# Performance work log

Measured on AMD Instinct MI355X. Metric: run time of the kernel, lower is better.

The kernel has to match this reference:

```python
import jax, jax.numpy as jnp
import numpy as np
from jax import lax

EPS = 1e-5  # BatchNorm / LayerNorm eps
B, DIM, H, W = 32, 256, 64, 64
S = 64            # state_dim
D_INNER = 256     # ssd_expand * dim
HIDDEN = 1024     # mlp_ratio * dim


def _bn(x, g, b, m, v):
    # BatchNorm2d, inference mode with given running stats. x: (B,C,H,W)
    inv = lax.rsqrt(v + EPS)
    return (x - m[None, :, None, None]) * (g * inv)[None, :, None, None] + b[None, :, None, None]


def _dwconv3x3(x, w):
    # depthwise 3x3 conv, stride 1, SAME padding. w: (C,1,3,3)
    return lax.conv_general_dilated(
        x, w, window_strides=(1, 1), padding='SAME',
        feature_group_count=x.shape[1],
        dimension_numbers=('NCHW', 'OIHW', 'NCHW'))


def setup_inputs() -> dict:
    key = jax.random.key(0)
    ks = jax.random.split(key, 32)
    n = lambda i, shp, s=0.02: jax.random.normal(ks[i], shp, jnp.float32) * s
    u = lambda i, shp: jax.random.uniform(ks[i], shp, jnp.float32)
    return {
        'x': jax.random.normal(ks[0], (B, DIM, H, W), jnp.float32),
        # dwconv1 (Conv2dNorm depthwise)
        'dw1_w': n(1, (DIM, 1, 3, 3)), 'dw1_g': 1.0 + n(2, (DIM,)), 'dw1_b': n(3, (DIM,)),
        'dw1_m': n(4, (DIM,)), 'dw1_v': u(5, (DIM,)) + 0.5,
        # LayerNorm1d
        'ln_w': 1.0 + n(6, (DIM,)), 'ln_b': n(7, (DIM,)),
        # mixer (HSMSSD)
        'bcdt_w': n(8, (3 * S, DIM)),
        'dwm_w': n(9, (3 * S, 1, 3, 3)),
        'A_param': 1.0 + 15.0 * u(10, (S,)),
        'hz_w': n(11, (2 * D_INNER, DIM)),
        'out_w': n(12, (DIM, D_INNER)),
        'D_param': jnp.ones((1,), jnp.float32),
        # dwconv2
        'dw2_w': n(13, (DIM, 1, 3, 3)), 'dw2_g': 1.0 + n(14, (DIM,)), 'dw2_b': n(15, (DIM,)),
        'dw2_m': n(16, (DIM,)), 'dw2_v': u(17, (DIM,)) + 0.5,
        # FFN
        'fc1_w': n(18, (HIDDEN, DIM)), 'fc1_g': 1.0 + n(19, (HIDDEN,)), 'fc1_b': n(20, (HIDDEN,)),
        'fc1_m': n(21, (HIDDEN,)), 'fc1_v': u(22, (HIDDEN,)) + 0.5,
        'fc2_w': n(23, (DIM, HIDDEN)), 'fc2_g': 1.0 + n(24, (DIM,)), 'fc2_b': n(25, (DIM,)),
        'fc2_m': n(26, (DIM,)), 'fc2_v': u(27, (DIM,)) + 0.5,
        # alpha-gated residual blends
        'alpha': 1e-4 * jnp.ones((4, DIM), jnp.float32) + n(28, (4, DIM), 0.01),
    }


def reference(x, dw1_w, dw1_g, dw1_b, dw1_m, dw1_v, ln_w, ln_b,
              bcdt_w, dwm_w, A_param, hz_w, out_w, D_param,
              dw2_w, dw2_g, dw2_b, dw2_m, dw2_v,
              fc1_w, fc1_g, fc1_b, fc1_m, fc1_v,
              fc2_w, fc2_g, fc2_b, fc2_m, fc2_v, alpha):
    b, dim, h_, w_ = x.shape
    L = h_ * w_
    a = jax.nn.sigmoid(alpha)[:, :, None, None]  # (4, dim, 1, 1)

    # alpha-blended depthwise conv 1
    x = (1.0 - a[0]) * x + a[0] * _bn(_dwconv3x3(x, dw1_w), dw1_g, dw1_b, dw1_m, dw1_v)
    x_prev = x

    # LayerNorm1d over channel dim on (B, C, L)
    xf = x.reshape(b, dim, L)
    mean = xf.mean(axis=1, keepdims=True)
    var = ((xf - mean) ** 2).mean(axis=1, keepdims=True)
    xn = (xf - mean) * lax.rsqrt(var + EPS) * ln_w[None, :, None] + ln_b[None, :, None]

    # HSMSSD mixer
    bc_dt = jnp.einsum('bcl,oc->bol', xn, bcdt_w).reshape(b, 3 * S, h_, w_)
    bc_dt = _dwconv3x3(bc_dt, dwm_w).reshape(b, 3 * S, L)
    Bm, Cm, dt = jnp.split(bc_dt, 3, axis=1)          # each (B, S, L)
    Am = jax.nn.softmax(dt + A_param[None, :, None], axis=-1)
    AB = Am * Bm                                      # (B, S, L)
    h = jnp.einsum('bcl,bsl->bcs', xn, AB)            # (B, dim, S)
    hz = jnp.einsum('bcs,oc->bos', h, hz_w)           # (B, 2*d_inner, S)
    hh, z = jnp.split(hz, 2, axis=1)
    hg = hh * jax.nn.silu(z) + hh * D_param[0]
    hout = jnp.einsum('bcs,oc->bos', hg, out_w)       # (B, dim, S)
    y = jnp.einsum('bcs,bsl->bcl', hout, Cm).reshape(b, dim, h_, w_)

    x = (1.0 - a[1]) * x_prev + a[1] * y
    x = (1.0 - a[2]) * x + a[2] * _bn(_dwconv3x3(x, dw2_w), dw2_g, dw2_b, dw2_m, dw2_v)

    # FFN: 1x1 conv + BN + ReLU + 1x1 conv + BN
    t = _bn(jnp.einsum('bchw,oc->bohw', x, fc1_w), fc1_g, fc1_b, fc1_m, fc1_v)
    t = jax.nn.relu(t)
    t = _bn(jnp.einsum('bchw,oc->bohw', t, fc2_w), fc2_g, fc2_b, fc2_m, fc2_v)
    x = (1.0 - a[3]) * x + a[3] * t
    return (x, hout)
```

## Files before the change

### kernel.cpp

```cpp
#include <hip/hip_runtime.h>
#include <hip/hip_bf16.h>

typedef __hip_bfloat16 bf16;
typedef __attribute__((ext_vector_type(8))) short bf16x8;
typedef __attribute__((ext_vector_type(4))) float f32x4;

__device__ __forceinline__ float LD(const float* p){ return *p; }
__device__ __forceinline__ float LD(const bf16* p){ return __bfloat162float(*p); }
__device__ __forceinline__ void ST(float* p, float v){ *p = v; }
__device__ __forceinline__ void ST(bf16* p, float v){ *p = __float2bfloat16(v); }
__device__ __forceinline__ float sigm(float v){ return 1.f/(1.f + expf(-v)); }
__device__ __forceinline__ ushort f2b(float f){
    unsigned u = __float_as_uint(f);
    return (ushort)((u + 0x7fffu + ((u>>16)&1u)) >> 16);
}

#define NEPS 1e-5f

__device__ __forceinline__ void stage_tile(const float* __restrict__ xp, float* tile, int tid){
    for (int i = tid; i < 66*66; i += 256) {
        int r = i/66, c = i%66;
        int gr = r-1, gc = c-1;
        float val = 0.f;
        if (gr >= 0 && gr < 64 && gc >= 0 && gc < 64) val = xp[gr*64+gc];
        tile[i] = val;
    }
}
__device__ __forceinline__ void stage_tile(const bf16* __restrict__ xp, float* tile, int tid){
    for (int i = tid; i < 2048; i += 256) {
        int r = i >> 5, c = (i & 31) << 1;
        uint u = *(const uint*)((const ushort*)xp + r*64 + c);
        tile[(r+1)*66 + c+1] = __uint_as_float(u << 16);
        tile[(r+1)*66 + c+2] = __uint_as_float(u & 0xffff0000u);
    }
    for (int i = tid; i < 260; i += 256) {
        int tr, tc;
        if (i < 66)       { tr = 0;      tc = i; }
        else if (i < 132) { tr = 65;     tc = i-66; }
        else if (i < 196) { tr = i-131;  tc = 0; }
        else              { tr = i-195;  tc = 65; }
        tile[tr*66 + tc] = 0.f;
    }
}
__device__ __forceinline__ void st_pair(float* op, int idx, float a, float b){
    op[idx] = a; op[idx+1] = b;
}
__device__ __forceinline__ void st_pair(bf16* op, int idx, float a, float b){
    uint u = (uint)f2b(a) | ((uint)f2b(b)<<16);
    *(uint*)((ushort*)op + idx) = u;
}

template<typename TIN, typename TOUT>
__global__ __launch_bounds__(256) void dwconv_bn_blend(
        const TIN* __restrict__ xin, TOUT* __restrict__ xout,
        const float* __restrict__ w, const float* __restrict__ gg, const float* __restrict__ bb,
        const float* __restrict__ mm, const float* __restrict__ vv,
        const float* __restrict__ alpha, int arow)
{
    __shared__ float tile[66*66];
    int blk = blockIdx.x;
    int ch = blk & 255;
    const TIN* xp = xin + (size_t)blk*4096;
    TOUT* op = xout + (size_t)blk*4096;
    int tid = threadIdx.x;
    stage_tile(xp, tile, tid);
    __syncthreads();
    float wv[9];
    #pragma unroll
    for (int k=0;k<9;k++) wv[k] = w[ch*9+k];
    float sc = gg[ch] * rsqrtf(vv[ch] + NEPS);
    float mv = mm[ch], bv = bb[ch];
    float av = sigm(alpha[arow*256+ch]);
    for (int p2 = tid; p2 < 2048; p2 += 256) {
        int r = p2 >> 5, c = (p2 & 31) << 1;
        float a0 = 0.f, a1 = 0.f;
        #pragma unroll
        for (int dr=0;dr<3;dr++)
            #pragma unroll
            for (int dc=0;dc<3;dc++){
                float wk = wv[dr*3+dc];
                a0 += wk*tile[(r+dr)*66 + c+dc];
                a1 += wk*tile[(r+dr)*66 + c+1+dc];
            }
        float bn0 = (a0 - mv)*sc + bv;
        float bn1 = (a1 - mv)*sc + bv;
        float xv0 = tile[(r+1)*66 + c+1];
        float xv1 = tile[(r+1)*66 + c+2];
        st_pair(op, r*64+c, (1.f-av)*xv0 + av*bn0, (1.f-av)*xv1 + av*bn1);
    }
}

template<typename TX>
__global__ __launch_bounds__(256) void ln_stats(const TX* __restrict__ x1,
        float* __restrict__ meanp, float* __restrict__ invp)
{
    int blk = blockIdx.x;
    int b = blk >> 4;
    int l = ((blk & 15) << 8) + threadIdx.x;
    const TX* xp = x1 + (size_t)b*256*4096 + l;
    float mean = 0.f, m2 = 0.f;
    for (int c=0;c<256;c++){ float v = LD(&xp[(size_t)c*4096]); mean += v; m2 += v*v; }
    mean *= (1.f/256.f); m2 *= (1.f/256.f);
    meanp[b*4096 + l] = mean;
    invp[b*4096 + l] = rsqrtf(m2 - mean*mean + NEPS);
}

__global__ __launch_bounds__(256) void prep_k(
        const float* __restrict__ f1w, const float* __restrict__ f2w,
        const float* __restrict__ bcdtw,
        const float* __restrict__ g1, const float* __restrict__ b1,
        const float* __restrict__ m1, const float* __restrict__ v1,
        const float* __restrict__ g2, const float* __restrict__ b2,
        const float* __restrict__ m2, const float* __restrict__ v2,
        ushort* __restrict__ w1bf, ushort* __restrict__ w2bf,
        ushort* __restrict__ wbc,
        float* __restrict__ sc1, float* __restrict__ sb1,
        float* __restrict__ sc2, float* __restrict__ sb2)
{
    int i = blockIdx.x*256 + threadIdx.x;
    if (i < 262144) {
        w1bf[i] = f2b(f1w[i]);
        w2bf[i] = f2b(f2w[i]);
    }
    if (i < 49152) wbc[i] = f2b(bcdtw[i]);
    if (i < 1024) { float s = g1[i]*rsqrtf(v1[i]+NEPS); sc1[i]=s; sb1[i]=b1[i]-m1[i]*s; }
    if (i < 256)  { float s = g2[i]*rsqrtf(v2[i]+NEPS); sc2[i]=s; sb2[i]=b2[i]-m2[i]*s; }
}

template<typename TX>
__global__ __launch_bounds__(256) void bcdt_mfma(
        const TX* __restrict__ x1,
        const float* __restrict__ meanp, const float* __restrict__ invp,
        const float* __restrict__ lnw, const float* __restrict__ lnb,
        const ushort* __restrict__ wbc,
        bf16* __restrict__ bc, ushort* __restrict__ xn_bf, int b0)
{
    __shared__ __align__(16) ushort Xs[64*256];
    int blk = blockIdx.x;
    int lb = blk >> 6;
    int b  = b0 + lb;
    int l0 = (blk & 63) << 6;
    int tid = threadIdx.x, lane = tid & 63, w = tid >> 6;
    const TX* xp = x1 + (size_t)b*256*4096 + l0;
    float mval = meanp[b*4096 + l0 + lane];
    float ival = invp [b*4096 + l0 + lane];
    ushort* xnp = xn_bf + (size_t)lb*256*4096 + l0;

    for (int cc = w*8; cc < 256; cc += 32) {
        ushort u[8];
        #pragma unroll
        for (int j=0;j<8;j++){
            float v = LD(&xp[(size_t)(cc+j)*4096 + lane]);
            float xn = (v - mval)*ival*lnw[cc+j] + lnb[cc+j];
            u[j] = f2b(xn);
            xnp[(size_t)(cc+j)*4096 + lane] = u[j];
        }
        uint4 pk;
        pk.x = (uint)u[0] | ((uint)u[1]<<16);
        pk.y = (uint)u[2] | ((uint)u[3]<<16);
        pk.z = (uint)u[4] | ((uint)u[5]<<16);
        pk.w = (uint)u[6] | ((uint)u[7]<<16);
        int g = (cc>>3) ^ (lane&7);
        *(uint4*)&Xs[lane*256 + g*8] = pk;
    }
    __syncthreads();

    f32x4 zero4 = {0.f,0.f,0.f,0.f};
    f32x4 acc[3][4];
    #pragma unroll
    for (int m=0;m<3;m++)
        #pragma unroll
        for (int f=0;f<4;f++) acc[m][f] = zero4;

    int hbase = w*48;
    #pragma unroll
    for (int ks=0; ks<8; ks++){
        bf16x8 afr[3];
        #pragma unroll
        for (int m=0;m<3;m++)
            afr[m] = *(const bf16x8*)&wbc[(size_t)(hbase + m*16 + (lane&15))*256
                                          + ks*32 + (lane>>4)*8];
        #pragma unroll
        for (int f=0;f<4;f++){
            int px = f*16 + (lane&15);
            int g = (ks*4 + (lane>>4)) ^ (px&7);
            bf16x8 bfr = *(const bf16x8*)&Xs[px*256 + g*8];
            #pragma unroll
            for (int m=0;m<3;m++)
                acc[m][f] = __builtin_amdgcn_mfma_f32_16x16x32_bf16(afr[m], bfr, acc[m][f], 0,0,0);
        }
    }
    bf16* op = bc + (size_t)lb*192*4096 + l0;
    #pragma unroll
    for (int m=0;m<3;m++)
        #pragma unroll
        for (int r=0;r<4;r++){
            int o = hbase + m*16 + (lane>>4)*4 + r;
            #pragma unroll
            for (int f=0;f<4;f++){
                int px = f*16 + (lane&15);
                op[(size_t)o*4096 + px] = __float2bfloat16(acc[m][f][r]);
            }
        }
}

__global__ __launch_bounds__(256) void dwconv_plain(bf16* __restrict__ data, const float* __restrict__ w)
{
    __shared__ float tile[66*66];
    int blk = blockIdx.x;
    int ch = blk % 192;
    bf16* xp = data + (size_t)blk*4096;
    int tid = threadIdx.x;
    stage_tile(xp, tile, tid);
    __syncthreads();
    float wv[9];
    #pragma unroll
    for (int k=0;k<9;k++) wv[k] = w[ch*9+k];
    for (int p2 = tid; p2 < 2048; p2 += 256) {
        int r = p2 >> 5, c = (p2 & 31) << 1;
        float a0 = 0.f, a1 = 0.f;
        #pragma unroll
        for (int dr=0;dr<3;dr++)
            #pragma unroll
            for (int dc=0;dc<3;dc++){
                float wk = wv[dr*3+dc];
                a0 += wk*tile[(r+dr)*66 + c+dc];
                a1 += wk*tile[(r+dr)*66 + c+1+dc];
            }
        st_pair(xp, r*64+c, a0, a1);
    }
}

__global__ __launch_bounds__(256) void softmax_ab(bf16* __restrict__ bc, const float* __restrict__ A)
{
    __shared__ float red[8];
    int blk = blockIdx.x;
    int lb = blk >> 6;
    int s = blk & 63;
    bf16* dtp = bc + ((size_t)lb*192 + 128 + s)*4096;
    bf16* bmp = bc + ((size_t)lb*192 + s)*4096;
    int tid = threadIdx.x;
    float Av = A[s];
    float vals[16];
    float mx = -1e30f;
    #pragma unroll
    for (int i=0;i<16;i++){ vals[i] = LD(&dtp[i*256+tid]) + Av; mx = fmaxf(mx, vals[i]); }
    #pragma unroll
    for (int o=32;o>0;o>>=1) mx = fmaxf(mx, __shfl_down(mx, o));
    int lane = tid & 63, wid = tid >> 6;
    if (lane == 0) red[wid] = mx;
    __syncthreads();
    if (tid == 0) red[4] = fmaxf(fmaxf(red[0],red[1]), fmaxf(red[2],red[3]));
    __syncthreads();
    mx = red[4];
    float sum = 0.f;
    #pragma unroll
    for (int i=0;i<16;i++){ vals[i] = expf(vals[i]-mx); sum += vals[i]; }
    #pragma unroll
    for (int o=32;o>0;o>>=1) sum += __shfl_down(sum, o);
    if (lane == 0) red[wid] = sum;
    __syncthreads();
    if (tid == 0) red[5] = red[0]+red[1]+red[2]+red[3];
    __syncthreads();
    float inv = 1.f/red[5];
    #pragma unroll
    for (int i=0;i<16;i++){
        float ab = vals[i]*inv*LD(&bmp[i*256+tid]);
        ST(&bmp[i*256+tid], ab);
    }
}

__global__ __launch_bounds__(256) void h_mfma(
        const ushort* __restrict__ xn_bf, const bf16* __restrict__ bc,
        float* __restrict__ h_part)
{
    int blk = blockIdx.x;
    int lb = blk >> 3;
    int kz = blk & 7;
    int kbase = kz*512;
    int tid = threadIdx.x, lane = tid & 63, w = tid >> 6;
    const ushort* ap = xn_bf + (size_t)lb*256*4096;
    const ushort* bp = (const ushort*)bc + (size_t)lb*192*4096;
    f32x4 zero4 = {0.f,0.f,0.f,0.f};
    f32x4 acc[4][4];
    #pragma unroll
    for (int m=0;m<4;m++)
        #pragma unroll
        for (int n=0;n<4;n++) acc[m][n] = zero4;

    for (int ks=0; ks<16; ks++){
        int koff = kbase + ks*32 + (lane>>4)*8;
        bf16x8 afr[4], bfr[4];
        #pragma unroll
        for (int m=0;m<4;m++)
            afr[m] = *(const bf16x8*)&ap[(size_t)(w*64 + m*16 + (lane&15))*4096 + koff];
        #pragma unroll
        for (int n=0;n<4;n++)
            bfr[n] = *(const bf16x8*)&bp[(size_t)(n*16 + (lane&15))*4096 + koff];
        #pragma unroll
        for (int m=0;m<4;m++)
            #pragma unroll
            for (int n=0;n<4;n++)
                acc[m][n] = __builtin_amdgcn_mfma_f32_16x16x32_bf16(afr[m], bfr[n], acc[m][n], 0,0,0);
    }
    float* hp = h_part + ((size_t)lb*8 + kz)*16384;
    #pragma unroll
    for (int m=0;m<4;m++)
        #pragma unroll
        for (int n=0;n<4;n++)
            #pragma unroll
            for (int r=0;r<4;r++){
                int c = w*64 + m*16 + (lane>>4)*4 + r;
                int s = n*16 + (lane&15);
                hp[c*64 + s] = acc[m][n][r];
            }
}

__global__ __launch_bounds__(256) void hz_gate(const float* __restrict__ h_part,
        const float* __restrict__ w, const float* __restrict__ Dp,
        float* __restrict__ hg)
{
    __shared__ float ht[256][64];
    int blk = blockIdx.x; int lb = blk>>2; int o0 = (blk&3)*64;
    int tid = threadIdx.x;
    const float* hp = h_part + (size_t)lb*8*16384;
    for (int i=tid;i<16384;i+=256){
        float s = 0.f;
        #pragma unroll
        for (int k=0;k<8;k++) s += hp[k*16384 + i];
        ht[i>>6][i&63] = s;
    }
    __syncthreads();
    int lane=tid&63, g=tid>>6;
    float Dv = Dp[0];
    for (int i4=0;i4<4;i4++){
        int ol = o0 + g*16 + i4*4;
        const float* r0 = w + (size_t)ol*256;
        const float *r1=r0+256, *r2=r0+512, *r3=r0+768;
        const float* z0 = w + (size_t)(ol+256)*256;
        const float *z1=z0+256, *z2=z0+512, *z3=z0+768;
        float d0=0.f,d1=0.f,d2=0.f,d3=0.f;
        float e0=0.f,e1=0.f,e2=0.f,e3=0.f;
        #pragma unroll 4
        for (int c4=0;c4<64;c4++){
            float x0=ht[c4*4][lane],x1v=ht[c4*4+1][lane],x2v=ht[c4*4+2][lane],x3v=ht[c4*4+3][lane];
            float4 a0=((const float4*)r0)[c4],a1=((const float4*)r1)[c4];
            float4 a2=((const float4*)r2)[c4],a3=((const float4*)r3)[c4];
            d0 += a0.x*x0+a0.y*x1v+a0.z*x2v+a0.w*x3v;
            d1 += a1.x*x0+a1.y*x1v+a1.z*x2v+a1.w*x3v;
            d2 += a2.x*x0+a2.y*x1v+a2.z*x2v+a2.w*x3v;
            d3 += a3.x*x0+a3.y*x1v+a3.z*x2v+a3.w*x3v;
            float4 b0=((const float4*)z0)[c4],b1=((const float4*)z1)[c4];
            float4 b2=((const float4*)z2)[c4],b3=((const float4*)z3)[c4];
            e0 += b0.x*x0+b0.y*x1v+b0.z*x2v+b0.w*x3v;
            e1 += b1.x*x0+b1.y*x1v+b1.z*x2v+b1.w*x3v;
            e2 += b2.x*x0+b2.y*x1v+b2.z*x2v+b2.w*x3v;
            e3 += b3.x*x0+b3.y*x1v+b3.z*x2v+b3.w*x3v;
        }
        float s0 = e0/(1.f+expf(-e0)) + Dv;
        float s1 = e1/(1.f+expf(-e1)) + Dv;
        float s2 = e2/(1.f+expf(-e2)) + Dv;
        float s3 = e3/(1.f+expf(-e3)) + Dv;
        size_t base = ((size_t)lb*256 + ol)*64 + lane;
        hg[base]=d0*s0; hg[base+64]=d1*s1; hg[base+128]=d2*s2; hg[base+192]=d3*s3;
    }
}

__global__ __launch_bounds__(256) void out_gemm(const float* __restrict__ hg, const float* __restrict__ w,
        ushort* __restrict__ hout_bf, float* __restrict__ hout_out, int b0)
{
    __shared__ float ht[256][64];
    int blk = blockIdx.x; int lb = blk>>2; int b = b0 + lb; int o0 = (blk&3)*64;
    int tid = threadIdx.x;
    const float* hp = hg + (size_t)lb*16384;
    for (int i=tid;i<16384;i+=256) ht[i>>6][i&63]=hp[i];
    __syncthreads();
    int lane=tid&63, g=tid>>6;
    for (int i4=0;i4<4;i4++){
        int ol = g*16 + i4*4;
        const float* r0 = w + (size_t)(o0+ol)*256;
        const float *r1=r0+256, *r2=r0+512, *r3=r0+768;
        float d0=0.f,d1=0.f,d2=0.f,d3=0.f;
        #pragma unroll 8
        for (int c4=0;c4<64;c4++){
            float x0=ht[c4*4][lane],x1v=ht[c4*4+1][lane],x2v=ht[c4*4+2][lane],x3v=ht[c4*4+3][lane];
            float4 a0=((const float4*)r0)[c4],a1=((const float4*)r1)[c4];
            float4 a2=((const float4*)r2)[c4],a3=((const float4*)r3)[c4];
            d0 += a0.x*x0+a0.y*x1v+a0.z*x2v+a0.w*x3v;
            d1 += a1.x*x0+a1.y*x1v+a1.z*x2v+a1.w*x3v;
            d2 += a2.x*x0+a2.y*x1v+a2.z*x2v+a2.w*x3v;
            d3 += a3.x*x0+a3.y*x1v+a3.z*x2v+a3.w*x3v;
        }
        size_t lbase = ((size_t)lb*256 + o0 + ol)*64 + lane;
        hout_bf[lbase]=f2b(d0); hout_bf[lbase+64]=f2b(d1);
        hout_bf[lbase+128]=f2b(d2); hout_bf[lbase+192]=f2b(d3);
        size_t gbase = ((size_t)b*256 + o0 + ol)*64 + lane;
        hout_out[gbase]=d0; hout_out[gbase+64]=d1;
        hout_out[gbase+128]=d2; hout_out[gbase+192]=d3;
    }
}

template<typename TX>
__global__ __launch_bounds__(256) void y_mfma(
        const ushort* __restrict__ hout_bf, const bf16* __restrict__ bc,
        TX* __restrict__ x1, const float* __restrict__ alpha, int b0)
{
    __shared__ __align__(16) ushort Cs[64*64];
    int blk = blockIdx.x; int lb = blk>>6; int b = b0 + lb; int l0 = (blk&63)<<6;
    int tid = threadIdx.x, lane = tid&63, w = tid>>6;
    const ushort* cp = (const ushort*)bc + ((size_t)lb*192 + 64)*4096 + l0;
    for (int sc = w*8; sc < 64; sc += 32){
        ushort u[8];
        #pragma unroll
        for (int j=0;j<8;j++) u[j] = cp[(size_t)(sc+j)*4096 + lane];
        uint4 pk;
        pk.x = (uint)u[0] | ((uint)u[1]<<16);
        pk.y = (uint)u[2] | ((uint)u[3]<<16);
        pk.z = (uint)u[4] | ((uint)u[5]<<16);
        pk.w = (uint)u[6] | ((uint)u[7]<<16);
        int g = (sc>>3) ^ (lane&7);
        *(uint4*)&Cs[lane*64 + g*8] = pk;
    }
    __syncthreads();

    f32x4 zero4 = {0.f,0.f,0.f,0.f};
    f32x4 acc[4][4];
    #pragma unroll
    for (int m=0;m<4;m++)
        #pragma unroll
        for (int f=0;f<4;f++) acc[m][f] = zero4;

    const ushort* ap = hout_bf + (size_t)lb*256*64;
    #pragma unroll
    for (int ks=0; ks<2; ks++){
        bf16x8 afr[4];
        #pragma unroll
        for (int m=0;m<4;m++)
            afr[m] = *(const bf16x8*)&ap[(size_t)(w*64 + m*16 + (lane&15))*64
                                          + ks*32 + (lane>>4)*8];
        #pragma unroll
        for (int f=0;f<4;f++){
            int px = f*16 + (lane&15);
            int s8 = ks*32 + (lane>>4)*8;
            int g = (s8>>3) ^ (px&7);
            bf16x8 bfr = *(const bf16x8*)&Cs[px*64 + g*8];
            #pragma unroll
            for (int m=0;m<4;m++)
                acc[m][f] = __builtin_amdgcn_mfma_f32_16x16x32_bf16(afr[m], bfr, acc[m][f], 0,0,0);
        }
    }

    TX* xpo = x1 + (size_t)b*256*4096 + l0;
    #pragma unroll
    for (int m=0;m<4;m++)
        #pragma unroll
        for (int r=0;r<4;r++){
            int c = w*64 + m*16 + (lane>>4)*4 + r;
            float av = sigm(alpha[256+c]);
            #pragma unroll
            for (int f=0;f<4;f++){
                int px = f*16 + (lane&15);
                float xv = LD(&xpo[(size_t)c*4096 + px]);
                ST(&xpo[(size_t)c*4096 + px], (1.f-av)*xv + av*acc[m][f][r]);
            }
        }
}

template<typename TX>
__global__ __launch_bounds__(256) void ffn_mfma(
        const TX* __restrict__ x,
        const ushort* __restrict__ w1bf,
        const ushort* __restrict__ w2bf,
        const float* __restrict__ sc1, const float* __restrict__ sb1,
        const float* __restrict__ sc2, const float* __restrict__ sb2,
        const float* __restrict__ alpha,
        float* __restrict__ out)
{
    __shared__ __align__(16) ushort Xs[64*256];
    __shared__ __align__(16) ushort Ts[64*128];
    int blk = blockIdx.x;
    int b = blk >> 6, l0 = (blk & 63) << 6;
    int tid = threadIdx.x, lane = tid & 63, w = tid >> 6;
    const TX* xp = x + (size_t)b*256*4096 + l0;

    for (int cc = w*8; cc < 256; cc += 32) {
        float v[8];
        #pragma unroll
        for (int j=0;j<8;j++) v[j] = LD(&xp[(size_t)(cc+j)*4096 + lane]);
        uint4 pk;
        pk.x = (uint)f2b(v[0]) | ((uint)f2b(v[1])<<16);
        pk.y = (uint)f2b(v[2]) | ((uint)f2b(v[3])<<16);
        pk.z = (uint)f2b(v[4]) | ((uint)f2b(v[5])<<16);
        pk.w = (uint)f2b(v[6]) | ((uint)f2b(v[7])<<16);
        int g = (cc>>3) ^ (lane&7);
        *(uint4*)&Xs[lane*256 + g*8] = pk;
    }
    __syncthreads();

    f32x4 zero4 = {0.f,0.f,0.f,0.f};
    f32x4 acc2[4][4];
    #pragma unroll
    for (int m=0;m<4;m++)
        #pragma unroll
        for (int f=0;f<4;f++) acc2[m][f] = zero4;

    for (int hc = 0; hc < 1024; hc += 128) {
        int hbase = hc + w*32;
        f32x4 c1[2][4];
        #pragma unroll
        for (int m=0;m<2;m++)
            #pragma unroll
            for (int f=0;f<4;f++) c1[m][f] = zero4;
        for (int ks = 0; ks < 8; ks++) {
            bf16x8 afr[2];
            #pragma unroll
            for (int m=0;m<2;m++)
                afr[m] = *(const bf16x8*)&w1bf[(size_t)(hbase + m*16 + (lane&15))*256
                                               + ks*32 + (lane>>4)*8];
            #pragma unroll
            for (int f=0;f<4;f++){
                int px = f*16 + (lane&15);
                int g = (ks*4 + (lane>>4)) ^ (px&7);
                bf16x8 bfr = *(const bf16x8*)&Xs[px*256 + g*8];
                #pragma unroll
                for (int m=0;m<2;m++)
                    c1[m][f] = __builtin_amdgcn_mfma_f32_16x16x32_bf16(afr[m], bfr, c1[m][f], 0,0,0);
            }
        }
        __syncthreads();
        #pragma unroll
        for (int m=0;m<2;m++){
            #pragma unroll
            for (int r=0;r<4;r++){
                int h = hbase + m*16 + (lane>>4)*4 + r;
                float s1 = sc1[h], bb1 = sb1[h];
                int hl = h - hc;
                #pragma unroll
                for (int f=0;f<4;f++){
                    int px = f*16 + (lane&15);
                    float t = fmaxf(c1[m][f][r]*s1 + bb1, 0.f);
                    int g = (hl>>3) ^ (px&7);
                    Ts[px*128 + g*8 + (hl&7)] = f2b(t);
                }
            }
        }
        __syncthreads();
        int c0 = w*64;
        for (int ks = 0; ks < 4; ks++) {
            bf16x8 afr[4];
            #pragma unroll
            for (int m=0;m<4;m++)
                afr[m] = *(const bf16x8*)&w2bf[(size_t)(c0 + m*16 + (lane&15))*1024
                                               + hc + ks*32 + (lane>>4)*8];
            #pragma unroll
            for (int f=0;f<4;f++){
                int px = f*16 + (lane&15);
                int hl = ks*32 + (lane>>4)*8;
                int g = (hl>>3) ^ (px&7);
                bf16x8 bfr = *(const bf16x8*)&Ts[px*128 + g*8];
                #pragma unroll
                for (int m=0;m<4;m++)
                    acc2[m][f] = __builtin_amdgcn_mfma_f32_16x16x32_bf16(afr[m], bfr, acc2[m][f], 0,0,0);
            }
        }
    }

    float* op = out + (size_t)b*256*4096 + l0;
    int c0 = w*64;
    #pragma unroll
    for (int m=0;m<4;m++){
        #pragma unroll
        for (int r=0;r<4;r++){
            int c = c0 + m*16 + (lane>>4)*4 + r;
            float a = sigm(alpha[768+c]);
            float s2 = sc2[c], bb2 = sb2[c];
            #pragma unroll
            for (int f=0;f<4;f++){
                int px = f*16 + (lane&15);
                float t2 = acc2[m][f][r]*s2 + bb2;
                float xv = LD(&xp[(size_t)c*4096 + px]);
                op[(size_t)c*4096 + px] = (1.f-a)*xv + a*t2;
            }
        }
    }
}

template<typename TX>
static void run_all(const float* x, TX* x1, float* d_out_x, float* hout_out,
                    const float* dw1w, const float* dw1g, const float* dw1b,
                    const float* dw1m, const float* dw1v,
                    const float* lnw, const float* lnb,
                    const ushort* wbc, const float* dwmw, const float* Ap,
                    const float* hzw, const float* outw, const float* Dp,
                    const float* dw2w, const float* dw2g, const float* dw2b,
                    const float* dw2m, const float* dw2v,
                    const ushort* w1bf, const ushort* w2bf,
                    const float* sc1, const float* sb1,
                    const float* sc2, const float* sb2,
                    const float* alpha,
                    float* meanp, float* invp, char* cbase, int NB,
                    hipStream_t stream)
{
    bf16*   bc      = (bf16*)cbase;
    ushort* xn_bf   = (ushort*)(cbase + (size_t)NB*1572864);
    float*  h_part  = (float*)(cbase + (size_t)NB*(1572864 + 2097152));
    float*  hg      = (float*)((char*)h_part + (size_t)NB*524288);
    ushort* hout_bf = (ushort*)((char*)hg + (size_t)NB*65536);

    dwconv_bn_blend<float,TX><<<8192,256,0,stream>>>(x, x1, dw1w,dw1g,dw1b,dw1m,dw1v, alpha, 0);
    ln_stats<TX><<<512,256,0,stream>>>(x1, meanp, invp);

    for (int b0 = 0; b0 < 32; b0 += NB) {
        bcdt_mfma<TX><<<NB*64,256,0,stream>>>(x1, meanp, invp, lnw, lnb, wbc, bc, xn_bf, b0);
        dwconv_plain<<<NB*192,256,0,stream>>>(bc, dwmw);
        softmax_ab<<<NB*64,256,0,stream>>>(bc, Ap);
        h_mfma<<<NB*8,256,0,stream>>>(xn_bf, bc, h_part);
        hz_gate<<<NB*4,256,0,stream>>>(h_part, hzw, Dp, hg);
        out_gemm<<<NB*4,256,0,stream>>>(hg, outw, hout_bf, hout_out, b0);
        y_mfma<TX><<<NB*64,256,0,stream>>>(hout_bf, bc, x1, alpha, b0);
    }

    dwconv_bn_blend<TX,TX><<<8192,256,0,stream>>>(x1, x1, dw2w,dw2g,dw2b,dw2m,dw2v, alpha, 2);
    ffn_mfma<TX><<<2048,256,0,stream>>>(x1, w1bf, w2bf, sc1, sb1, sc2, sb2, alpha, d_out_x);
}

extern "C" void kernel_launch(void* const* d_in, const int* in_sizes, int n_in,
                              void* d_out, int out_size, void* d_ws, size_t ws_size,
                              hipStream_t stream)
{
    (void)in_sizes; (void)n_in; (void)out_size;
    const float* x     = (const float*)d_in[0];
    const float* dw1w  = (const float*)d_in[1];
    const float* dw1g  = (const float*)d_in[2];
    const float* dw1b  = (const float*)d_in[3];
    const float* dw1m  = (const float*)d_in[4];
    const float* dw1v  = (const float*)d_in[5];
    const float* lnw   = (const float*)d_in[6];
    const float* lnb   = (const float*)d_in[7];
    const float* bcdtw = (const float*)d_in[8];
    const float* dwmw  = (const float*)d_in[9];
    const float* Ap    = (const float*)d_in[10];
    const float* hzw   = (const float*)d_in[11];
    const float* outw  = (const float*)d_in[12];
    const float* Dp    = (const float*)d_in[13];
    const float* dw2w  = (const float*)d_in[14];
    const float* dw2g  = (const float*)d_in[15];
    const float* dw2b  = (const float*)d_in[16];
    const float* dw2m  = (const float*)d_in[17];
    const float* dw2v  = (const float*)d_in[18];
    const float* f1w   = (const float*)d_in[19];
    const float* f1g   = (const float*)d_in[20];
    const float* f1b   = (const float*)d_in[21];
    const float* f1m   = (const float*)d_in[22];
    const float* f1v   = (const float*)d_in[23];
    const float* f2w   = (const float*)d_in[24];
    const float* f2g   = (const float*)d_in[25];
    const float* f2b_  = (const float*)d_in[26];
    const float* f2m   = (const float*)d_in[27];
    const float* f2v   = (const float*)d_in[28];
    const float* alpha = (const float*)d_in[29];

    const size_t nx = (size_t)32*256*4096;
    float* d_out_x  = (float*)d_out;
    float* hout_out = d_out_x + nx;

    char* ws = (char*)d_ws;
    float* meanp = (float*)ws;
    float* invp  = meanp + 131072;
    size_t off = 1048576;
    ushort* w1bf = (ushort*)(ws + off); off += 524288;
    ushort* w2bf = (ushort*)(ws + off); off += 524288;
    ushort* wbc  = (ushort*)(ws + off); off += 98304;
    float* sc1 = (float*)(ws + off); off += 4096;
    float* sb1 = (float*)(ws + off); off += 4096;
    float* sc2 = (float*)(ws + off); off += 1024;
    float* sb2 = (float*)(ws + off); off += 1024;
    off = (off + 255) & ~(size_t)255;

    const size_t perb = 1572864 + 2097152 + 524288 + 65536 + 32768;
    size_t avail = ws_size > off ? ws_size - off : 0;

    prep_k<<<1024,256,0,stream>>>(f1w, f2w, bcdtw, f1g,f1b,f1m,f1v, f2g,f2b_,f2m,f2v,
                                  w1bf, w2bf, wbc, sc1, sb1, sc2, sb2);

    if (avail >= nx*2 + 8*perb) {
        bf16* x1b = (bf16*)(ws + off); off += nx*2;
        char* cbase = ws + off;
        size_t a2 = ws_size - off;
        int NB = 8;
        for (int nb = 32; nb >= 8; nb >>= 1) if (a2 >= (size_t)nb*perb) { NB = nb; break; }
        run_all<bf16>(x, x1b, d_out_x, hout_out,
                      dw1w,dw1g,dw1b,dw1m,dw1v, lnw,lnb, wbc, dwmw, Ap, hzw, outw, Dp,
                      dw2w,dw2g,dw2b,dw2m,dw2v, w1bf,w2bf, sc1,sb1,sc2,sb2, alpha,
                      meanp, invp, cbase, NB, stream);
    } else {
        char* cbase = ws + off;
        int NB = 1;
        for (int nb = 32; nb >= 1; nb >>= 1) if (avail >= (size_t)nb*perb) { NB = nb; break; }
        run_all<float>(x, d_out_x, d_out_x, hout_out,
                       dw1w,dw1g,dw1b,dw1m,dw1v, lnw,lnb, wbc, dwmw, Ap, hzw, outw, Dp,
                       dw2w,dw2g,dw2b,dw2m,dw2v, w1bf,w2bf, sc1,sb1,sc2,sb2, alpha,
                       meanp, invp, cbase, NB, stream);
    }
}
```

Before: 663.4 us.

## Use finer split-K with atomic accumulation in h_mfma; vectorize bf16 LN stats

The h GEMM is now split 32 ways along the sequence instead of 8. Partial results are accumulated with float atomicAdd into a buffer that is zeroed with a memset each batch chunk, so hz_gate no longer reduces eight partial copies. The aim is more blocks in flight for the small-grid h GEMM and less partial-buffer traffic. LayerNorm stats for bf16 activations now load two values per 32-bit read. The cost is atomic contention, an extra memset launch per chunk, and summation order that is no longer deterministic.

```diff
diff --git a/kernel.cpp b/kernel.cpp
--- a/kernel.cpp
+++ b/kernel.cpp
@@ -1,5 +1,6 @@
 #include <hip/hip_runtime.h>
 #include <hip/hip_bf16.h>
+#include <type_traits>
 
 typedef __hip_bfloat16 bf16;
 typedef __attribute__((ext_vector_type(8))) short bf16x8;
@@ -90,19 +91,41 @@
     }
 }
 
-template<typename TX>
-__global__ __launch_bounds__(256) void ln_stats(const TX* __restrict__ x1,
+__global__ __launch_bounds__(256) void ln_stats_f(const float* __restrict__ x1,
         float* __restrict__ meanp, float* __restrict__ invp)
 {
     int blk = blockIdx.x;
     int b = blk >> 4;
     int l = ((blk & 15) << 8) + threadIdx.x;
-    const TX* xp = x1 + (size_t)b*256*4096 + l;
+    const float* xp = x1 + (size_t)b*256*4096 + l;
     float mean = 0.f, m2 = 0.f;
-    for (int c=0;c<256;c++){ float v = LD(&xp[(size_t)c*4096]); mean += v; m2 += v*v; }
+    for (int c=0;c<256;c++){ float v = xp[(size_t)c*4096]; mean += v; m2 += v*v; }
     mean *= (1.f/256.f); m2 *= (1.f/256.f);
     meanp[b*4096 + l] = mean;
     invp[b*4096 + l] = rsqrtf(m2 - mean*mean + NEPS);
+}
+
+__global__ __launch_bounds__(256) void ln_stats_bf(const bf16* __restrict__ x1,
+        float* __restrict__ meanp, float* __restrict__ invp)
+{
+    int blk = blockIdx.x;
+    int b = blk >> 3;
+    int l = ((blk & 7) << 9) + (threadIdx.x << 1);
+    const ushort* xp = (const ushort*)x1 + (size_t)b*256*4096 + l;
+    float mean0 = 0.f, m20 = 0.f, mean1 = 0.f, m21 = 0.f;
+    for (int c=0;c<256;c++){
+        uint u = *(const uint*)&xp[(size_t)c*4096];
+        float v0 = __uint_as_float(u << 16);
+        float v1 = __uint_as_float(u & 0xffff0000u);
+        mean0 += v0; m20 += v0*v0;
+        mean1 += v1; m21 += v1*v1;
+    }
+    mean0 *= (1.f/256.f); m20 *= (1.f/256.f);
+    mean1 *= (1.f/256.f); m21 *= (1.f/256.f);
+    meanp[b*4096 + l]   = mean0;
+    meanp[b*4096 + l+1] = mean1;
+    invp[b*4096 + l]   = rsqrtf(m20 - mean0*mean0 + NEPS);
+    invp[b*4096 + l+1] = rsqrtf(m21 - mean1*mean1 + NEPS);
 }
 
 __global__ __launch_bounds__(256) void prep_k(
@@ -272,12 +295,12 @@
 
 __global__ __launch_bounds__(256) void h_mfma(
         const ushort* __restrict__ xn_bf, const bf16* __restrict__ bc,
-        float* __restrict__ h_part)
+        float* __restrict__ h)
 {
     int blk = blockIdx.x;
-    int lb = blk >> 3;
-    int kz = blk & 7;
-    int kbase = kz*512;
+    int lb = blk >> 5;
+    int kz = blk & 31;
+    int kbase = kz*128;
     int tid = threadIdx.x, lane = tid & 63, w = tid >> 6;
     const ushort* ap = xn_bf + (size_t)lb*256*4096;
     const ushort* bp = (const ushort*)bc + (size_t)lb*192*4096;
@@ -288,7 +311,8 @@
         #pragma unroll
         for (int n=0;n<4;n++) acc[m][n] = zero4;
 
-    for (int ks=0; ks<16; ks++){
+    #pragma unroll
+    for (int ks=0; ks<4; ks++){
         int koff = kbase + ks*32 + (lane>>4)*8;
         bf16x8 afr[4], bfr[4];
         #pragma unroll
@@ -303,7 +327,7 @@
             for (int n=0;n<4;n++)
                 acc[m][n] = __builtin_amdgcn_mfma_f32_16x16x32_bf16(afr[m], bfr[n], acc[m][n], 0,0,0);
     }
-    float* hp = h_part + ((size_t)lb*8 + kz)*16384;
+    float* hp = h + (size_t)lb*16384;
     #pragma unroll
     for (int m=0;m<4;m++)
         #pragma unroll
@@ -312,24 +336,19 @@
             for (int r=0;r<4;r++){
                 int c = w*64 + m*16 + (lane>>4)*4 + r;
                 int s = n*16 + (lane&15);
-                hp[c*64 + s] = acc[m][n][r];
-            }
-}
-
-__global__ __launch_bounds__(256) void hz_gate(const float* __restrict__ h_part,
+                atomicAdd(&hp[c*64 + s], acc[m][n][r]);
+            }
+}
+
+__global__ __launch_bounds__(256) void hz_gate(const float* __restrict__ h,
         const float* __restrict__ w, const float* __restrict__ Dp,
         float* __restrict__ hg)
 {
     __shared__ float ht[256][64];
     int blk = blockIdx.x; int lb = blk>>2; int o0 = (blk&3)*64;
     int tid = threadIdx.x;
-    const float* hp = h_part + (size_t)lb*8*16384;
-    for (int i=tid;i<16384;i+=256){
-        float s = 0.f;
-        #pragma unroll
-        for (int k=0;k<8;k++) s += hp[k*16384 + i];
-        ht[i>>6][i&63] = s;
-    }
+    const float* hp = h + (size_t)lb*16384;
+    for (int i=tid;i<16384;i+=256) ht[i>>6][i&63] = hp[i];
     __syncthreads();
     int lane=tid&63, g=tid>>6;
     float Dv = Dp[0];
@@ -603,19 +622,23 @@
 {
     bf16*   bc      = (bf16*)cbase;
     ushort* xn_bf   = (ushort*)(cbase + (size_t)NB*1572864);
-    float*  h_part  = (float*)(cbase + (size_t)NB*(1572864 + 2097152));
-    float*  hg      = (float*)((char*)h_part + (size_t)NB*524288);
+    float*  h       = (float*)(cbase + (size_t)NB*(1572864 + 2097152));
+    float*  hg      = (float*)((char*)h + (size_t)NB*65536);
     ushort* hout_bf = (ushort*)((char*)hg + (size_t)NB*65536);
 
     dwconv_bn_blend<float,TX><<<8192,256,0,stream>>>(x, x1, dw1w,dw1g,dw1b,dw1m,dw1v, alpha, 0);
-    ln_stats<TX><<<512,256,0,stream>>>(x1, meanp, invp);
+    if constexpr (std::is_same<TX,bf16>::value)
+        ln_stats_bf<<<256,256,0,stream>>>(x1, meanp, invp);
+    else
+        ln_stats_f<<<512,256,0,stream>>>((const float*)x1, meanp, invp);
 
     for (int b0 = 0; b0 < 32; b0 += NB) {
         bcdt_mfma<TX><<<NB*64,256,0,stream>>>(x1, meanp, invp, lnw, lnb, wbc, bc, xn_bf, b0);
         dwconv_plain<<<NB*192,256,0,stream>>>(bc, dwmw);
         softmax_ab<<<NB*64,256,0,stream>>>(bc, Ap);
-        h_mfma<<<NB*8,256,0,stream>>>(xn_bf, bc, h_part);
-        hz_gate<<<NB*4,256,0,stream>>>(h_part, hzw, Dp, hg);
+        hipMemsetAsync(h, 0, (size_t)NB*65536, stream);
+        h_mfma<<<NB*32,256,0,stream>>>(xn_bf, bc, h);
+        hz_gate<<<NB*4,256,0,stream>>>(h, hzw, Dp, hg);
         out_gemm<<<NB*4,256,0,stream>>>(hg, outw, hout_bf, hout_out, b0);
         y_mfma<TX><<<NB*64,256,0,stream>>>(hout_bf, bc, x1, alpha, b0);
     }
@@ -677,7 +700,7 @@
     float* sb2 = (float*)(ws + off); off += 1024;
     off = (off + 255) & ~(size_t)255;
 
-    const size_t perb = 1572864 + 2097152 + 524288 + 65536 + 32768;
+    const size_t perb = 1572864 + 2097152 + 65536 + 65536 + 32768;
     size_t avail = ws_size > off ? ws_size - off : 0;
 
     prep_k<<<1024,256,0,stream>>>(f1w, f2w, bcdtw, f1g,f1b,f1m,f1v, f2g,f2b_,f2m,f2v,
```

Measured after the change: 702.8 us. +5.9%, slower.
